# Kernel tuning notes

Measured on AMD Instinct MI355X. Metric: run time of the kernel, lower is better.

## Reference

```python
import jax, jax.numpy as jnp
import numpy as np

N = 50000       # nodes
E = 800000      # edges before self-loops (avg degree 16)
D_IN = 128
D_OUT = 128
DELTA = 2.5     # scaler normalization
EPS = 1e-5      # batchnorm eps
NEG_SLOPE = 0.01  # LeakyReLU default


def _lin_init(k, fan_in, shape):
    s = 1.0 / np.sqrt(fan_in)
    return jax.random.uniform(k, shape, jnp.float32, -s, s)


def setup_inputs() -> dict:
    key = jax.random.key(0)
    ks = jax.random.split(key, 12)
    ndata = jax.random.normal(ks[0], (N, D_IN), jnp.float32)
    src = jax.random.randint(ks[1], (E,), 0, N, jnp.int32)
    dst = jax.random.randint(ks[2], (E,), 0, N, jnp.int32)
    # PNAConvTower.M : Linear(2*in, in)
    M_w = _lin_init(ks[3], 2 * D_IN, (2 * D_IN, D_IN))
    M_b = _lin_init(ks[4], 2 * D_IN, (D_IN,))
    # PNAConvTower.U : Linear((3 aggs * 2 scalers + 1)*in, out) = Linear(7*in, out)
    U_w = _lin_init(ks[5], 7 * D_IN, (7 * D_IN, D_OUT))
    U_b = _lin_init(ks[6], 7 * D_IN, (D_OUT,))
    bn_gamma = jnp.ones((D_OUT,), jnp.float32)
    bn_beta = jnp.zeros((D_OUT,), jnp.float32)
    # PNAConv mixing layer: Linear(out, out) + LeakyReLU
    mix_w = _lin_init(ks[7], D_OUT, (D_OUT, D_OUT))
    mix_b = _lin_init(ks[8], D_OUT, (D_OUT,))
    return dict(ndata=ndata, M_w=M_w, M_b=M_b, U_w=U_w, U_b=U_b,
                bn_gamma=bn_gamma, bn_beta=bn_beta, mix_w=mix_w, mix_b=mix_b,
                src=src, dst=dst)


def reference(ndata, M_w, M_b, U_w, U_b, bn_gamma, bn_beta, mix_w, mix_b, src, dst):
    n = ndata.shape[0]
    # dgl.add_self_loop: append (i, i) for every node
    loop = jnp.arange(n, dtype=src.dtype)
    s = jnp.concatenate([src, loop])
    d = jnp.concatenate([dst, loop])
    # per-edge message: M(cat[h_src, h_dst])
    msg = jnp.concatenate([ndata[s], ndata[d]], axis=-1) @ M_w + M_b  # (E+N, D_IN)
    # in-degree per destination (>=1 due to self loops)
    deg = jax.ops.segment_sum(jnp.ones(d.shape, jnp.float32), d, num_segments=n)  # (N,)
    mean_agg = jax.ops.segment_sum(msg, d, num_segments=n) / deg[:, None]
    max_agg = jax.ops.segment_max(msg, d, num_segments=n)
    # aggregators ['mean','max','mean'] concatenated along feature dim
    agg = jnp.concatenate([mean_agg, max_agg, mean_agg], axis=-1)  # (N, 3*D_IN)
    # scalers ['identity','amplification'] applied to the concatenation
    amp = (jnp.log(deg + 1.0) / DELTA)[:, None]
    h_neigh = jnp.concatenate([agg, agg * amp], axis=-1)  # (N, 6*D_IN)
    # post-transform U on cat[node_feat, h_neigh]
    h = jnp.concatenate([ndata, h_neigh], axis=-1) @ U_w + U_b  # (N, D_OUT)
    # BatchNorm1d (training-mode batch stats, biased var)
    mu = h.mean(axis=0)
    var = ((h - mu) ** 2).mean(axis=0)
    h = (h - mu) * jax.lax.rsqrt(var + EPS) * bn_gamma + bn_beta
    # mixing layer: Linear + LeakyReLU
    out = h @ mix_w + mix_b
    return jax.nn.leaky_relu(out, NEG_SLOPE)
```

## Files before the change

kernel.cpp:

```cpp
#include <hip/hip_runtime.h>
#include <hip/hip_bf16.h>

#define NN 50000
#define EE 800000
#define DD 128

typedef short bf8 __attribute__((ext_vector_type(8)));
typedef float f32x4 __attribute__((ext_vector_type(4)));

__device__ __forceinline__ unsigned short f2b(float f) {
  __hip_bfloat16 h = __float2bfloat16(f);
  return *reinterpret_cast<unsigned short*>(&h);
}

__device__ __forceinline__ bf8 mk_a(const float* __restrict__ p, float sc) {
  float4 x0 = *(const float4*)p;
  float4 x1 = *(const float4*)(p + 4);
  bf8 a;
  a[0] = (short)f2b(x0.x * sc); a[1] = (short)f2b(x0.y * sc);
  a[2] = (short)f2b(x0.z * sc); a[3] = (short)f2b(x0.w * sc);
  a[4] = (short)f2b(x1.x * sc); a[5] = (short)f2b(x1.y * sc);
  a[6] = (short)f2b(x1.z * sc); a[7] = (short)f2b(x1.w * sc);
  return a;
}


__global__ __launch_bounds__(256) void pack_prep(const float* __restrict__ Mw,
                                                 unsigned short* __restrict__ Mp) {
  int gid = blockIdx.x * 256 + threadIdx.x;
  if (gid >= 32768) return;
  int j = gid & 7, l = (gid >> 3) & 63, ct = (gid >> 9) & 15, kt = gid >> 13;
  int k = kt * 32 + ((l >> 4) << 3) + j;
  int c = ct * 16 + (l & 15);
  float v = (c < 128) ? Mw[k * DD + c] : Mw[(128 + k) * DD + (c - 128)];
  Mp[gid] = f2b(v);
}

__global__ __launch_bounds__(256) void pack_u(const float* __restrict__ Uw,
                                              unsigned short* __restrict__ Up) {
  int gid = blockIdx.x * 256 + threadIdx.x;
  if (gid >= 81920) return;
  int j = gid & 7, l = (gid >> 3) & 63, ct = (gid >> 9) & 7, kt = gid >> 12;
  int k = kt * 32 + ((l >> 4) << 3) + j;
  int p = k >> 7, kk = k & 127;
  int c = ct * 16 + (l & 15);
  float v;
  switch (p) {
    case 0: v = Uw[kk * DD + c]; break;
    case 1: v = Uw[(128 + kk) * DD + c] + Uw[(384 + kk) * DD + c]; break;
    case 2: v = Uw[(512 + kk) * DD + c] + Uw[(768 + kk) * DD + c]; break;
    case 3: v = Uw[(256 + kk) * DD + c]; break;
    default: v = Uw[(640 + kk) * DD + c]; break;
  }
  Up[gid] = f2b(v);
}

__global__ __launch_bounds__(256) void pack_mix(const float* __restrict__ Mixw,
                                                unsigned short* __restrict__ Xp) {
  int gid = blockIdx.x * 256 + threadIdx.x;
  if (gid >= 16384) return;
  int j = gid & 7, l = (gid >> 3) & 63, ct = (gid >> 9) & 7, kt = gid >> 12;
  int k = kt * 32 + ((l >> 4) << 3) + j;
  int c = ct * 16 + (l & 15);
  Xp[gid] = f2b(Mixw[k * DD + c]);
}

__global__ __launch_bounds__(256) void gemm_prep(
    const float* __restrict__ nd, const unsigned short* __restrict__ Mp,
    const float* __restrict__ Mb, float* __restrict__ A, float* __restrict__ Bv) {
  const int w = threadIdx.x >> 6, l = threadIdx.x & 63;
  const int half = w >> 1;
  const int row0 = blockIdx.x * 32 + (w & 1) * 16;
  const int rc = min(row0 + (l & 15), NN - 1);
  const int ko = (l >> 4) * 8;
  const bf8* B8 = (const bf8*)Mp;
  f32x4 zero = {0.f, 0.f, 0.f, 0.f};
  f32x4 acc[8];
  #pragma unroll
  for (int i = 0; i < 8; i++) acc[i] = zero;
  #pragma unroll
  for (int ks = 0; ks < 4; ks++) {
    bf8 a = mk_a(nd + (size_t)rc * DD + ks * 32 + ko, 1.f);
    #pragma unroll
    for (int ct = 0; ct < 8; ct++) {
      bf8 b = B8[(ks * 16 + half * 8 + ct) * 64 + l];
      acc[ct] = __builtin_amdgcn_mfma_f32_16x16x32_bf16(a, b, acc[ct], 0, 0, 0);
    }
  }
  const int rb = row0 + (l >> 4) * 4;
  float* outp = half ? Bv : A;
  #pragma unroll
  for (int ct = 0; ct < 8; ct++) {
    int c = ct * 16 + (l & 15);
    float bias = half ? Mb[c] : 0.f;
    #pragma unroll
    for (int jj = 0; jj < 4; jj++) {
      int rr = rb + jj;
      if (rr < NN) outp[(size_t)rr * DD + c] = acc[ct][jj] + bias;
    }
  }
}

__global__ __launch_bounds__(256) void init_small(
    unsigned int* __restrict__ cnt, float* __restrict__ bns, float* __restrict__ bnq) {
  int i = blockIdx.x * 256 + threadIdx.x;
  if (i < NN) cnt[i] = 0u;
  if (i < DD) { bns[i] = 0.f; bnq[i] = 0.f; }
}

__global__ __launch_bounds__(256) void deg_count(
    const int* __restrict__ dst, unsigned int* __restrict__ cnt) {
  int e = blockIdx.x * 256 + threadIdx.x;
  if (e < EE) atomicAdd(&cnt[dst[e]], 1u);
}

__global__ __launch_bounds__(1024) void scan_k(
    const unsigned int* __restrict__ cnt, unsigned int* __restrict__ off,
    unsigned int* __restrict__ cursor) {
  __shared__ unsigned int part[1024];
  const int t = threadIdx.x;
  const int CH = (NN + 1023) / 1024;
  int beg = t * CH, end = beg + CH;
  if (end > NN) end = NN;
  unsigned int s = 0;
  for (int i = beg; i < end; i++) s += cnt[i];
  part[t] = s;
  __syncthreads();
  for (int d = 1; d < 1024; d <<= 1) {
    unsigned int v = (t >= d) ? part[t - d] : 0u;
    __syncthreads();
    part[t] += v;
    __syncthreads();
  }
  unsigned int run = part[t] - s;
  for (int i = beg; i < end; i++) {
    off[i] = run; cursor[i] = run; run += cnt[i];
  }
  if (t == 0) off[NN] = EE;
}

__global__ __launch_bounds__(256) void fill_k(
    const int* __restrict__ src, const int* __restrict__ dst,
    unsigned int* __restrict__ cursor, unsigned int* __restrict__ eidx) {
  int e = blockIdx.x * 256 + threadIdx.x;
  if (e < EE) {
    unsigned int p = atomicAdd(&cursor[dst[e]], 1u);
    eidx[p] = (unsigned int)src[e];
  }
}

__global__ __launch_bounds__(256) void aggregate(
    const float* __restrict__ A, const float* __restrict__ Bv,
    const unsigned int* __restrict__ off, const unsigned int* __restrict__ eidx,
    float* __restrict__ S, float* __restrict__ Xm, float* __restrict__ amp) {
  int wave = threadIdx.x >> 6, lane = threadIdx.x & 63;
  int n = blockIdx.x * 4 + wave;
  if (n >= NN) return;
  unsigned int b0 = off[n], b1 = off[n + 1];
  float2 sum = ((const float2*)(A + (size_t)n * DD))[lane];
  float2 mx = sum;
  for (unsigned int j0 = b0; j0 < b1; j0 += 64) {
    int m = (int)min(64u, b1 - j0);
    int myi = (lane < m) ? (int)eidx[j0 + lane] : 0;
    for (int j = 0; j < m; j++) {
      int sN = __shfl(myi, j);
      float2 a = ((const float2*)(A + (size_t)sN * DD))[lane];
      sum.x += a.x; sum.y += a.y;
      mx.x = fmaxf(mx.x, a.x); mx.y = fmaxf(mx.y, a.y);
    }
  }
  float degf = (float)(b1 - b0) + 1.f;
  float inv = 1.f / degf;
  float2 b = ((const float2*)(Bv + (size_t)n * DD))[lane];
  float2 sm = {sum.x * inv + b.x, sum.y * inv + b.y};
  float2 xm = {mx.x + b.x, mx.y + b.y};
  ((float2*)(S + (size_t)n * DD))[lane] = sm;
  ((float2*)(Xm + (size_t)n * DD))[lane] = xm;
  if (lane == 0) amp[n] = logf(degf + 1.f) * 0.4f;
}

__global__ __launch_bounds__(256) void gemm_u(
    const float* __restrict__ nd, const float* __restrict__ S, const float* __restrict__ Xm,
    const float* __restrict__ amp, const unsigned short* __restrict__ Up,
    const float* __restrict__ Ub, float* __restrict__ H) {
  const int w = threadIdx.x >> 6, l = threadIdx.x & 63;
  const int row0 = blockIdx.x * 64 + w * 16;
  const int rc = min(row0 + (l & 15), NN - 1);
  const int ko = (l >> 4) * 8;
  const float av = amp[rc];
  const bf8* B8 = (const bf8*)Up;
  f32x4 zero = {0.f, 0.f, 0.f, 0.f};
  f32x4 acc[8];
  #pragma unroll
  for (int i = 0; i < 8; i++) acc[i] = zero;

  #pragma unroll 1
  for (int p = 0; p < 5; p++) {
    const float* sp = (p == 0) ? nd : (p < 3) ? S : Xm;
    const float sc = (p == 2 || p == 4) ? av : 1.f;
    const float* base = sp + (size_t)rc * DD + ko;
    #pragma unroll
    for (int q = 0; q < 4; q++) {
      bf8 a = mk_a(base + q * 32, sc);
      const int ks = p * 4 + q;
      #pragma unroll
      for (int ct = 0; ct < 8; ct++) {
        bf8 b = B8[(ks * 8 + ct) * 64 + l];
        acc[ct] = __builtin_amdgcn_mfma_f32_16x16x32_bf16(a, b, acc[ct], 0, 0, 0);
      }
    }
  }
  const int rb = row0 + (l >> 4) * 4;
  #pragma unroll
  for (int ct = 0; ct < 8; ct++) {
    int c = ct * 16 + (l & 15);
    float ub = Ub[c];
    #pragma unroll
    for (int jj = 0; jj < 4; jj++) {
      int rr = rb + jj;
      if (rr < NN) H[(size_t)rr * DD + c] = acc[ct][jj] + ub;
    }
  }
}

__global__ __launch_bounds__(256) void bn_stats(
    const float* __restrict__ H, float* __restrict__ bns, float* __restrict__ bnq) {
  int c = threadIdx.x & 127, g = threadIdx.x >> 7;
  float s = 0.f, q = 0.f;
  for (int n = blockIdx.x * 2 + g; n < NN; n += gridDim.x * 2) {
    float v = H[n * DD + c];
    s += v; q += v * v;
  }
  atomicAdd(bns + c, s);
  atomicAdd(bnq + c, q);
}

__global__ __launch_bounds__(128) void bn_finalize(
    const float* __restrict__ bns, const float* __restrict__ bnq,
    const float* __restrict__ gamma, const float* __restrict__ beta,
    float* __restrict__ bnA, float* __restrict__ bnO) {
  int c = threadIdx.x;
  float mu = bns[c] * (1.f / NN);
  float var = bnq[c] * (1.f / NN) - mu * mu;
  float a = gamma[c] * rsqrtf(var + 1e-5f);
  bnA[c] = a;
  bnO[c] = beta[c] - mu * a;
}

__global__ __launch_bounds__(256) void gemm_final(
    const float* __restrict__ H, const float* __restrict__ bnA, const float* __restrict__ bnO,
    const unsigned short* __restrict__ Xp, const float* __restrict__ mixb,
    float* __restrict__ out) {
  const int w = threadIdx.x >> 6, l = threadIdx.x & 63;
  const int row0 = blockIdx.x * 64 + w * 16;
  const int rc = min(row0 + (l & 15), NN - 1);
  const int ko = (l >> 4) * 8;
  const bf8* B8 = (const bf8*)Xp;
  f32x4 zero = {0.f, 0.f, 0.f, 0.f};
  f32x4 acc[8];
  #pragma unroll
  for (int i = 0; i < 8; i++) acc[i] = zero;

  #pragma unroll
  for (int ks = 0; ks < 4; ks++) {
    const float* p = H + (size_t)rc * DD + ks * 32 + ko;
    float4 x0 = *(const float4*)p;
    float4 x1 = *(const float4*)(p + 4);
    float4 a0 = *(const float4*)(bnA + ks * 32 + ko);
    float4 a1 = *(const float4*)(bnA + ks * 32 + ko + 4);
    float4 o0 = *(const float4*)(bnO + ks * 32 + ko);
    float4 o1 = *(const float4*)(bnO + ks * 32 + ko + 4);
    bf8 a;
    a[0] = (short)f2b(x0.x * a0.x + o0.x); a[1] = (short)f2b(x0.y * a0.y + o0.y);
    a[2] = (short)f2b(x0.z * a0.z + o0.z); a[3] = (short)f2b(x0.w * a0.w + o0.w);
    a[4] = (short)f2b(x1.x * a1.x + o1.x); a[5] = (short)f2b(x1.y * a1.y + o1.y);
    a[6] = (short)f2b(x1.z * a1.z + o1.z); a[7] = (short)f2b(x1.w * a1.w + o1.w);
    #pragma unroll
    for (int ct = 0; ct < 8; ct++) {
      bf8 b = B8[(ks * 8 + ct) * 64 + l];
      acc[ct] = __builtin_amdgcn_mfma_f32_16x16x32_bf16(a, b, acc[ct], 0, 0, 0);
    }
  }
  const int rb = row0 + (l >> 4) * 4;
  #pragma unroll
  for (int ct = 0; ct < 8; ct++) {
    int c = ct * 16 + (l & 15);
    float mbv = mixb[c];
    #pragma unroll
    for (int jj = 0; jj < 4; jj++) {
      int rr = rb + jj;
      if (rr < NN) {
        float o = acc[ct][jj] + mbv;
        o = o > 0.f ? o : 0.01f * o;
        out[(size_t)rr * DD + c] = o;
      }
    }
  }
}

extern "C" void kernel_launch(void* const* d_in, const int* in_sizes, int n_in,
                              void* d_out, int out_size, void* d_ws, size_t ws_size,
                              hipStream_t stream) {
  const float* nd    = (const float*)d_in[0];
  const float* Mw    = (const float*)d_in[1];
  const float* Mb    = (const float*)d_in[2];
  const float* Uw    = (const float*)d_in[3];
  const float* Ub    = (const float*)d_in[4];
  const float* gamma = (const float*)d_in[5];
  const float* beta  = (const float*)d_in[6];
  const float* mixw  = (const float*)d_in[7];
  const float* mixb  = (const float*)d_in[8];
  const int* src = (const int*)d_in[9];
  const int* dst = (const int*)d_in[10];
  float* out = (float*)d_out;

  float* ws  = (float*)d_ws;
  float* A   = ws;
  float* Bv  = A + (size_t)NN * DD;
  float* S   = Bv + (size_t)NN * DD;
  float* Xm  = S + (size_t)NN * DD;
  float* H   = Xm + (size_t)NN * DD;
  float* amp = H + (size_t)NN * DD;
  float* bns = amp + NN;
  float* bnq = bns + DD;
  float* bnA = bnq + DD;
  float* bnO = bnA + DD;
  unsigned short* Mp = (unsigned short*)(bnO + DD);
  unsigned short* Up = Mp + 32768;
  unsigned short* Xp = Up + 81920;
  unsigned int* cnt    = (unsigned int*)(Xp + 16384);
  unsigned int* off    = cnt + NN;
  unsigned int* cursor = off + NN + 1;
  unsigned int* eidx   = cursor + NN;

  pack_prep<<<128, 256, 0, stream>>>(Mw, Mp);
  pack_u<<<320, 256, 0, stream>>>(Uw, Up);
  pack_mix<<<64, 256, 0, stream>>>(mixw, Xp);

  gemm_prep<<<(NN + 31) / 32, 256, 0, stream>>>(nd, Mp, Mb, A, Bv);

  init_small<<<(NN + 255) / 256, 256, 0, stream>>>(cnt, bns, bnq);
  deg_count<<<(EE + 255) / 256, 256, 0, stream>>>(dst, cnt);
  scan_k<<<1, 1024, 0, stream>>>(cnt, off, cursor);
  fill_k<<<(EE + 255) / 256, 256, 0, stream>>>(src, dst, cursor, eidx);
  aggregate<<<(NN + 3) / 4, 256, 0, stream>>>(A, Bv, off, eidx, S, Xm, amp);

  gemm_u<<<(NN + 63) / 64, 256, 0, stream>>>(nd, S, Xm, amp, Up, Ub, H);
  bn_stats<<<500, 256, 0, stream>>>(H, bns, bnq);
  bn_finalize<<<1, 128, 0, stream>>>(bns, bnq, gamma, beta, bnA, bnO);
  gemm_final<<<(NN + 63) / 64, 256, 0, stream>>>(H, bnA, bnO, Xp, mixb, out);
}
```

Before: 512.5 us.

## Merge pack/init kernels, parallelize CSR scan, fuse BN stats into GEMMs

Merges the three weight-packing kernels and the zero-init into one launch. Replaces the single-block serial scan with a three-kernel block-parallel scan. Moves the batch-norm statistics into the gemm_u epilogue using wave shuffles and atomics, and recomputes the BN scale and offset inside gemm_final. This removes two kernel launches and a full re-read of H, at the cost of more atomics and redundant per-thread BN math, and per-block atomic float sums that are order-nondeterministic.

```diff
diff --git a/kernel.cpp b/kernel.cpp
--- a/kernel.cpp
+++ b/kernel.cpp
@@ -4,6 +4,7 @@
 #define NN 50000
 #define EE 800000
 #define DD 128
+#define NBLK_SCAN 196
 
 typedef short bf8 __attribute__((ext_vector_type(8)));
 typedef float f32x4 __attribute__((ext_vector_type(4)));
@@ -24,45 +25,43 @@
   return a;
 }
 
-
-__global__ __launch_bounds__(256) void pack_prep(const float* __restrict__ Mw,
-                                                 unsigned short* __restrict__ Mp) {
+__global__ __launch_bounds__(256) void pack_all(
+    const float* __restrict__ Mw, const float* __restrict__ Uw, const float* __restrict__ Mixw,
+    unsigned short* __restrict__ Mp, unsigned short* __restrict__ Up,
+    unsigned short* __restrict__ Xp, unsigned int* __restrict__ cnt,
+    float* __restrict__ bns, float* __restrict__ bnq) {
   int gid = blockIdx.x * 256 + threadIdx.x;
-  if (gid >= 32768) return;
-  int j = gid & 7, l = (gid >> 3) & 63, ct = (gid >> 9) & 15, kt = gid >> 13;
-  int k = kt * 32 + ((l >> 4) << 3) + j;
-  int c = ct * 16 + (l & 15);
-  float v = (c < 128) ? Mw[k * DD + c] : Mw[(128 + k) * DD + (c - 128)];
-  Mp[gid] = f2b(v);
-}
-
-__global__ __launch_bounds__(256) void pack_u(const float* __restrict__ Uw,
-                                              unsigned short* __restrict__ Up) {
-  int gid = blockIdx.x * 256 + threadIdx.x;
-  if (gid >= 81920) return;
-  int j = gid & 7, l = (gid >> 3) & 63, ct = (gid >> 9) & 7, kt = gid >> 12;
-  int k = kt * 32 + ((l >> 4) << 3) + j;
-  int p = k >> 7, kk = k & 127;
-  int c = ct * 16 + (l & 15);
-  float v;
-  switch (p) {
-    case 0: v = Uw[kk * DD + c]; break;
-    case 1: v = Uw[(128 + kk) * DD + c] + Uw[(384 + kk) * DD + c]; break;
-    case 2: v = Uw[(512 + kk) * DD + c] + Uw[(768 + kk) * DD + c]; break;
-    case 3: v = Uw[(256 + kk) * DD + c]; break;
-    default: v = Uw[(640 + kk) * DD + c]; break;
-  }
-  Up[gid] = f2b(v);
-}
-
-__global__ __launch_bounds__(256) void pack_mix(const float* __restrict__ Mixw,
-                                                unsigned short* __restrict__ Xp) {
-  int gid = blockIdx.x * 256 + threadIdx.x;
-  if (gid >= 16384) return;
-  int j = gid & 7, l = (gid >> 3) & 63, ct = (gid >> 9) & 7, kt = gid >> 12;
-  int k = kt * 32 + ((l >> 4) << 3) + j;
-  int c = ct * 16 + (l & 15);
-  Xp[gid] = f2b(Mixw[k * DD + c]);
+  if (gid < NN) cnt[gid] = 0u;
+  if (gid < DD) { bns[gid] = 0.f; bnq[gid] = 0.f; }
+  if (gid < 32768) {
+    int g = gid;
+    int j = g & 7, l = (g >> 3) & 63, ct = (g >> 9) & 15, kt = g >> 13;
+    int k = kt * 32 + ((l >> 4) << 3) + j;
+    int c = ct * 16 + (l & 15);
+    float v = (c < 128) ? Mw[k * DD + c] : Mw[(128 + k) * DD + (c - 128)];
+    Mp[g] = f2b(v);
+  } else if (gid < 32768 + 81920) {
+    int g = gid - 32768;
+    int j = g & 7, l = (g >> 3) & 63, ct = (g >> 9) & 7, kt = g >> 12;
+    int k = kt * 32 + ((l >> 4) << 3) + j;
+    int p = k >> 7, kk = k & 127;
+    int c = ct * 16 + (l & 15);
+    float v;
+    switch (p) {
+      case 0: v = Uw[kk * DD + c]; break;
+      case 1: v = Uw[(128 + kk) * DD + c] + Uw[(384 + kk) * DD + c]; break;
+      case 2: v = Uw[(512 + kk) * DD + c] + Uw[(768 + kk) * DD + c]; break;
+      case 3: v = Uw[(256 + kk) * DD + c]; break;
+      default: v = Uw[(640 + kk) * DD + c]; break;
+    }
+    Up[g] = f2b(v);
+  } else if (gid < 131072) {
+    int g = gid - 114688;
+    int j = g & 7, l = (g >> 3) & 63, ct = (g >> 9) & 7, kt = g >> 12;
+    int k = kt * 32 + ((l >> 4) << 3) + j;
+    int c = ct * 16 + (l & 15);
+    Xp[g] = f2b(Mixw[k * DD + c]);
+  }
 }
 
 __global__ __launch_bounds__(256) void gemm_prep(
@@ -101,42 +100,56 @@
   }
 }
 
-__global__ __launch_bounds__(256) void init_small(
-    unsigned int* __restrict__ cnt, float* __restrict__ bns, float* __restrict__ bnq) {
-  int i = blockIdx.x * 256 + threadIdx.x;
-  if (i < NN) cnt[i] = 0u;
-  if (i < DD) { bns[i] = 0.f; bnq[i] = 0.f; }
-}
-
 __global__ __launch_bounds__(256) void deg_count(
     const int* __restrict__ dst, unsigned int* __restrict__ cnt) {
   int e = blockIdx.x * 256 + threadIdx.x;
   if (e < EE) atomicAdd(&cnt[dst[e]], 1u);
 }
 
-__global__ __launch_bounds__(1024) void scan_k(
-    const unsigned int* __restrict__ cnt, unsigned int* __restrict__ off,
-    unsigned int* __restrict__ cursor) {
-  __shared__ unsigned int part[1024];
+__global__ __launch_bounds__(256) void scan_blk(
+    const unsigned int* __restrict__ cnt, unsigned int* __restrict__ loc,
+    unsigned int* __restrict__ bsum) {
+  __shared__ unsigned int sh[256];
   const int t = threadIdx.x;
-  const int CH = (NN + 1023) / 1024;
-  int beg = t * CH, end = beg + CH;
-  if (end > NN) end = NN;
-  unsigned int s = 0;
-  for (int i = beg; i < end; i++) s += cnt[i];
-  part[t] = s;
+  const int i = blockIdx.x * 256 + t;
+  unsigned int v = (i < NN) ? cnt[i] : 0u;
+  sh[t] = v;
   __syncthreads();
-  for (int d = 1; d < 1024; d <<= 1) {
-    unsigned int v = (t >= d) ? part[t - d] : 0u;
+  for (int d = 1; d < 256; d <<= 1) {
+    unsigned int u = (t >= d) ? sh[t - d] : 0u;
     __syncthreads();
-    part[t] += v;
+    sh[t] += u;
     __syncthreads();
   }
-  unsigned int run = part[t] - s;
-  for (int i = beg; i < end; i++) {
-    off[i] = run; cursor[i] = run; run += cnt[i];
-  }
-  if (t == 0) off[NN] = EE;
+  if (i < NN) loc[i] = sh[t] - v;
+  if (t == 255) bsum[blockIdx.x] = sh[255];
+}
+
+__global__ __launch_bounds__(256) void scan_top(
+    const unsigned int* __restrict__ bsum, unsigned int* __restrict__ bbase) {
+  __shared__ unsigned int sh[256];
+  const int t = threadIdx.x;
+  unsigned int v = (t < NBLK_SCAN) ? bsum[t] : 0u;
+  sh[t] = v;
+  __syncthreads();
+  for (int d = 1; d < 256; d <<= 1) {
+    unsigned int u = (t >= d) ? sh[t - d] : 0u;
+    __syncthreads();
+    sh[t] += u;
+    __syncthreads();
+  }
+  if (t < NBLK_SCAN) bbase[t] = sh[t] - v;
+}
+
+__global__ __launch_bounds__(256) void scan_fin(
+    const unsigned int* __restrict__ loc, const unsigned int* __restrict__ bbase,
+    unsigned int* __restrict__ off, unsigned int* __restrict__ cursor) {
+  const int i = blockIdx.x * 256 + threadIdx.x;
+  if (i < NN) {
+    unsigned int o = loc[i] + bbase[blockIdx.x];
+    off[i] = o; cursor[i] = o;
+  }
+  if (i == 0) off[NN] = EE;
 }
 
 __global__ __launch_bounds__(256) void fill_k(
@@ -182,7 +195,8 @@
 __global__ __launch_bounds__(256) void gemm_u(
     const float* __restrict__ nd, const float* __restrict__ S, const float* __restrict__ Xm,
     const float* __restrict__ amp, const unsigned short* __restrict__ Up,
-    const float* __restrict__ Ub, float* __restrict__ H) {
+    const float* __restrict__ Ub, float* __restrict__ H,
+    float* __restrict__ bns, float* __restrict__ bnq) {
   const int w = threadIdx.x >> 6, l = threadIdx.x & 63;
   const int row0 = blockIdx.x * 64 + w * 16;
   const int rc = min(row0 + (l & 15), NN - 1);
@@ -215,40 +229,28 @@
   for (int ct = 0; ct < 8; ct++) {
     int c = ct * 16 + (l & 15);
     float ub = Ub[c];
+    float sS = 0.f, sQ = 0.f;
     #pragma unroll
     for (int jj = 0; jj < 4; jj++) {
       int rr = rb + jj;
-      if (rr < NN) H[(size_t)rr * DD + c] = acc[ct][jj] + ub;
-    }
-  }
-}
-
-__global__ __launch_bounds__(256) void bn_stats(
-    const float* __restrict__ H, float* __restrict__ bns, float* __restrict__ bnq) {
-  int c = threadIdx.x & 127, g = threadIdx.x >> 7;
-  float s = 0.f, q = 0.f;
-  for (int n = blockIdx.x * 2 + g; n < NN; n += gridDim.x * 2) {
-    float v = H[n * DD + c];
-    s += v; q += v * v;
-  }
-  atomicAdd(bns + c, s);
-  atomicAdd(bnq + c, q);
-}
-
-__global__ __launch_bounds__(128) void bn_finalize(
-    const float* __restrict__ bns, const float* __restrict__ bnq,
+      if (rr < NN) {
+        float h = acc[ct][jj] + ub;
+        H[(size_t)rr * DD + c] = h;
+        sS += h; sQ += h * h;
+      }
+    }
+    sS += __shfl_xor(sS, 16); sS += __shfl_xor(sS, 32);
+    sQ += __shfl_xor(sQ, 16); sQ += __shfl_xor(sQ, 32);
+    if ((l >> 4) == 0) {
+      atomicAdd(bns + c, sS);
+      atomicAdd(bnq + c, sQ);
+    }
+  }
+}
+
+__global__ __launch_bounds__(256) void gemm_final(
+    const float* __restrict__ H, const float* __restrict__ bns, const float* __restrict__ bnq,
     const float* __restrict__ gamma, const float* __restrict__ beta,
-    float* __restrict__ bnA, float* __restrict__ bnO) {
-  int c = threadIdx.x;
-  float mu = bns[c] * (1.f / NN);
-  float var = bnq[c] * (1.f / NN) - mu * mu;
-  float a = gamma[c] * rsqrtf(var + 1e-5f);
-  bnA[c] = a;
-  bnO[c] = beta[c] - mu * a;
-}
-
-__global__ __launch_bounds__(256) void gemm_final(
-    const float* __restrict__ H, const float* __restrict__ bnA, const float* __restrict__ bnO,
     const unsigned short* __restrict__ Xp, const float* __restrict__ mixb,
     float* __restrict__ out) {
   const int w = threadIdx.x >> 6, l = threadIdx.x & 63;
@@ -256,25 +258,37 @@
   const int rc = min(row0 + (l & 15), NN - 1);
   const int ko = (l >> 4) * 8;
   const bf8* B8 = (const bf8*)Xp;
+  const float invN = 1.f / (float)NN;
   f32x4 zero = {0.f, 0.f, 0.f, 0.f};
   f32x4 acc[8];
   #pragma unroll
   for (int i = 0; i < 8; i++) acc[i] = zero;
 
+  float aA[8], aO[8];
   #pragma unroll
   for (int ks = 0; ks < 4; ks++) {
-    const float* p = H + (size_t)rc * DD + ks * 32 + ko;
+    const int kch = ks * 32 + ko;
+    if (ks == 0) {}
+  }
+  #pragma unroll
+  for (int ks = 0; ks < 4; ks++) {
+    const int kch = ks * 32 + ko;
+    #pragma unroll
+    for (int j = 0; j < 8; j++) {
+      int c = kch + j;
+      float mu = bns[c] * invN;
+      float var = bnq[c] * invN - mu * mu;
+      float a = gamma[c] * rsqrtf(var + 1e-5f);
+      aA[j] = a; aO[j] = beta[c] - mu * a;
+    }
+    const float* p = H + (size_t)rc * DD + kch;
     float4 x0 = *(const float4*)p;
     float4 x1 = *(const float4*)(p + 4);
-    float4 a0 = *(const float4*)(bnA + ks * 32 + ko);
-    float4 a1 = *(const float4*)(bnA + ks * 32 + ko + 4);
-    float4 o0 = *(const float4*)(bnO + ks * 32 + ko);
-    float4 o1 = *(const float4*)(bnO + ks * 32 + ko + 4);
     bf8 a;
-    a[0] = (short)f2b(x0.x * a0.x + o0.x); a[1] = (short)f2b(x0.y * a0.y + o0.y);
-    a[2] = (short)f2b(x0.z * a0.z + o0.z); a[3] = (short)f2b(x0.w * a0.w + o0.w);
-    a[4] = (short)f2b(x1.x * a1.x + o1.x); a[5] = (short)f2b(x1.y * a1.y + o1.y);
-    a[6] = (short)f2b(x1.z * a1.z + o1.z); a[7] = (short)f2b(x1.w * a1.w + o1.w);
+    a[0] = (short)f2b(x0.x * aA[0] + aO[0]); a[1] = (short)f2b(x0.y * aA[1] + aO[1]);
+    a[2] = (short)f2b(x0.z * aA[2] + aO[2]); a[3] = (short)f2b(x0.w * aA[3] + aO[3]);
+    a[4] = (short)f2b(x1.x * aA[4] + aO[4]); a[5] = (short)f2b(x1.y * aA[5] + aO[5]);
+    a[6] = (short)f2b(x1.z * aA[6] + aO[6]); a[7] = (short)f2b(x1.w * aA[7] + aO[7]);
     #pragma unroll
     for (int ct = 0; ct < 8; ct++) {
       bf8 b = B8[(ks * 8 + ct) * 64 + l];
@@ -323,30 +337,25 @@
   float* amp = H + (size_t)NN * DD;
   float* bns = amp + NN;
   float* bnq = bns + DD;
-  float* bnA = bnq + DD;
-  float* bnO = bnA + DD;
-  unsigned short* Mp = (unsigned short*)(bnO + DD);
+  unsigned short* Mp = (unsigned short*)(bnq + DD);
   unsigned short* Up = Mp + 32768;
   unsigned short* Xp = Up + 81920;
   unsigned int* cnt    = (unsigned int*)(Xp + 16384);
   unsigned int* off    = cnt + NN;
   unsigned int* cursor = off + NN + 1;
   unsigned int* eidx   = cursor + NN;
-
-  pack_prep<<<128, 256, 0, stream>>>(Mw, Mp);
-  pack_u<<<320, 256, 0, stream>>>(Uw, Up);
-  pack_mix<<<64, 256, 0, stream>>>(mixw, Xp);
-
+  unsigned int* loc    = eidx + EE;
+  unsigned int* bsum   = loc + NN;
+  unsigned int* bbase  = bsum + 256;
+
+  pack_all<<<512, 256, 0, stream>>>(Mw, Uw, mixw, Mp, Up, Xp, cnt, bns, bnq);
   gemm_prep<<<(NN + 31) / 32, 256, 0, stream>>>(nd, Mp, Mb, A, Bv);
-
-  init_small<<<(NN + 255) / 256, 256, 0, stream>>>(cnt, bns, bnq);
   deg_count<<<(EE + 255) / 256, 256, 0, stream>>>(dst, cnt);
-  scan_k<<<1, 1024, 0, stream>>>(cnt, off, cursor);
+  scan_blk<<<NBLK_SCAN, 256, 0, stream>>>(cnt, loc, bsum);
+  scan_top<<<1, 256, 0, stream>>>(bsum, bbase);
+  scan_fin<<<NBLK_SCAN, 256, 0, stream>>>(loc, bbase, off, cursor);
   fill_k<<<(EE + 255) / 256, 256, 0, stream>>>(src, dst, cursor, eidx);
   aggregate<<<(NN + 3) / 4, 256, 0, stream>>>(A, Bv, off, eidx, S, Xm, amp);
-
-  gemm_u<<<(NN + 63) / 64, 256, 0, stream>>>(nd, S, Xm, amp, Up, Ub, H);
-  bn_stats<<<500, 256, 0, stream>>>(H, bns, bnq);
-  bn_finalize<<<1, 128, 0, stream>>>(bns, bnq, gamma, beta, bnA, bnO);
-  gemm_final<<<(NN + 63) / 64, 256, 0, stream>>>(H, bnA, bnO, Xp, mixb, out);
-}
+  gemm_u<<<(NN + 63) / 64, 256, 0, stream>>>(nd, S, Xm, amp, Up, Ub, H, bns, bnq);
+  gemm_final<<<(NN + 63) / 64, 256, 0, stream>>>(H, bns, bnq, gamma, beta, Xp, mixb, out);
+}
```

Result: faster. 479.7 us (-6.4%).
